# Kernel optimization log

Measured on AMD Instinct MI355X. Metric: run time of the kernel, lower is better.

The kernel has to match this reference:

```python
import jax, jax.numpy as jnp
import numpy as np

V = 50257   # vocab_size
BLK = 2048  # block_size
L = 4       # n_layer
H = 12      # n_head
C = 768     # n_embd
B, T = 2, 2048
EPS = 1e-5


def _ln(x, w):
    # LayerNorm without bias (config.bias=False)
    m = x.mean(-1, keepdims=True)
    v = ((x - m) ** 2).mean(-1, keepdims=True)
    return (x - m) * jax.lax.rsqrt(v + EPS) * w


def setup_inputs() -> dict:
    key = jax.random.key(0)
    ks = jax.random.split(key, 12)
    s = 0.02  # init std, matches _init_weights
    inp = {
        "idx": jax.random.randint(ks[0], (B, T), 0, V),
        "targets": jax.random.randint(ks[1], (B, T), 0, V),
        "wte": jax.random.normal(ks[2], (V, C), jnp.float32) * s,
        "wpe": jax.random.normal(ks[3], (BLK, C), jnp.float32) * s,
        # per-layer stacked params; linear weights stored as [in, out] (x @ W)
        "ln1_w": jnp.ones((L, C), jnp.float32),
        "attn_w": jax.random.normal(ks[4], (L, C, 3 * C), jnp.float32) * s,
        "attn_proj_w": jax.random.normal(ks[5], (L, C, C), jnp.float32) * s,
        "ln2_w": jnp.ones((L, C), jnp.float32),
        "fc_w": jax.random.normal(ks[6], (L, C, 4 * C), jnp.float32) * s,
        "mlp_proj_w": jax.random.normal(ks[7], (L, 4 * C, C), jnp.float32) * s,
        "lnf_w": jnp.ones((C,), jnp.float32),
        "lm_head_w": jax.random.normal(ks[8], (C, V), jnp.float32) * s,
    }
    return inp


def reference(idx, targets, wte, wpe, ln1_w, attn_w, attn_proj_w, ln2_w,
              fc_w, mlp_proj_w, lnf_w, lm_head_w):
    b, t = idx.shape
    hd = C // H
    x = wte[idx] + wpe[:t]  # [B,T,C] (dropout=0.0)
    mask = jnp.tril(jnp.ones((t, t), bool))

    def block(x, p):
        ln1w, Wqkv, Wo, ln2w, Wfc, Wp = p
        h = _ln(x, ln1w)
        qkv = h @ Wqkv  # [B,T,3C]
        q, k, v = jnp.split(qkv, 3, axis=-1)
        to_heads = lambda z: z.reshape(b, t, H, hd).transpose(0, 2, 1, 3)  # [B,H,T,hd]
        q, k, v = to_heads(q), to_heads(k), to_heads(v)
        att = jnp.einsum('bhqd,bhkd->bhqk', q, k) * (1.0 / np.sqrt(hd))
        att = jnp.where(mask, att, -jnp.inf)
        att = jax.nn.softmax(att, axis=-1)
        y = jnp.einsum('bhqk,bhkd->bhqd', att, v)
        y = y.transpose(0, 2, 1, 3).reshape(b, t, C)
        x = x + y @ Wo
        h2 = _ln(x, ln2w)
        x = x + jax.nn.gelu(h2 @ Wfc, approximate=False) @ Wp
        return x, None

    x, _ = jax.lax.scan(block, x, (ln1_w, attn_w, attn_proj_w, ln2_w, fc_w, mlp_proj_w))
    x = _ln(x, lnf_w)
    logits = x @ lm_head_w  # [B,T,V]
    logp = jax.nn.log_softmax(logits, axis=-1)
    loss = -jnp.take_along_axis(logp, targets[..., None], axis=-1).mean()
    return logits, loss
```

## Files before the change

kernel.cpp:

```cpp
#include <hip/hip_runtime.h>
#include <math.h>


#define TT 2048
#define CC 768
#define HH 12
#define HD 64
#define VV 50257
#define BBATCH 2
#define ROWS (BBATCH * TT)
#define LMSTRIP 8192

typedef __attribute__((ext_vector_type(8))) short short8;
typedef __attribute__((ext_vector_type(4))) float floatx4;

typedef const void __attribute__((address_space(1)))* gas1_cvp;
typedef void __attribute__((address_space(3)))* as3_vp;

static __device__ __forceinline__ void gload_lds16(const void* g, void* l) {
  __builtin_amdgcn_global_load_lds(
      (gas1_cvp)(unsigned long long)g,
      (as3_vp)(unsigned int)(unsigned long long)l, 16, 0, 0);
}

static __device__ __forceinline__ ushort f2bf(float x) {
  unsigned u = __float_as_uint(x);
  unsigned r = (u + 0x7fff + ((u >> 16) & 1)) >> 16;
  return (ushort)r;
}
static __device__ __forceinline__ float bf2f(ushort h) {
  return __uint_as_float(((unsigned)h) << 16);
}

static __device__ __forceinline__ void xcd_swizzle(int gx, int gy, int& bx, int& by) {
  int nwg = gx * gy;
  int orig = by * gx + bx;
  int q = nwg >> 3, r = nwg & 7;
  int xcd = orig & 7, local = orig >> 3;
  int wgid = (xcd < r ? xcd * (q + 1) : r * (q + 1) + (xcd - r) * q) + local;
  bx = wgid % gx;
  by = wgid / gx;
}

__global__ void embed_kernel(const int* __restrict__ idx,
                             const float* __restrict__ wte,
                             const float* __restrict__ wpe,
                             float* __restrict__ x) {
  int i = blockIdx.x * blockDim.x + threadIdx.x;
  int row = i / (CC / 4);
  int c4 = (i % (CC / 4)) * 4;
  int t = row % TT;
  int tok = idx[row];
  float4 a = *(const float4*)(wte + (size_t)tok * CC + c4);
  float4 p = *(const float4*)(wpe + (size_t)t * CC + c4);
  float4 o;
  o.x = a.x + p.x; o.y = a.y + p.y; o.z = a.z + p.z; o.w = a.w + p.w;
  *(float4*)(x + (size_t)row * CC + c4) = o;
}

__global__ void ln_split_kernel(const float* __restrict__ x,
                                const float* __restrict__ w,
                                ushort* __restrict__ hhi,
                                ushort* __restrict__ hlo) {
  int wid = threadIdx.x >> 6;
  int lane = threadIdx.x & 63;
  int row = blockIdx.x * 4 + wid;
  const float* xr = x + (size_t)row * CC;
  float v[12];
#pragma unroll
  for (int c = 0; c < 3; c++) {
    float4 t = *(const float4*)(xr + c * 256 + lane * 4);
    v[c * 4 + 0] = t.x; v[c * 4 + 1] = t.y; v[c * 4 + 2] = t.z; v[c * 4 + 3] = t.w;
  }
  float s = 0.f;
#pragma unroll
  for (int i = 0; i < 12; i++) s += v[i];
#pragma unroll
  for (int o = 32; o > 0; o >>= 1) s += __shfl_xor(s, o);
  float mean = s * (1.0f / CC);
  float vs = 0.f;
#pragma unroll
  for (int i = 0; i < 12; i++) { float d = v[i] - mean; vs += d * d; }
#pragma unroll
  for (int o = 32; o > 0; o >>= 1) vs += __shfl_xor(vs, o);
  float rs = rsqrtf(vs * (1.0f / CC) + 1e-5f);
#pragma unroll
  for (int c = 0; c < 3; c++) {
    float4 wv = *(const float4*)(w + c * 256 + lane * 4);
    float r[4];
    r[0] = (v[c * 4 + 0] - mean) * rs * wv.x;
    r[1] = (v[c * 4 + 1] - mean) * rs * wv.y;
    r[2] = (v[c * 4 + 2] - mean) * rs * wv.z;
    r[3] = (v[c * 4 + 3] - mean) * rs * wv.w;
    ushort4 h, l;
    h.x = f2bf(r[0]); l.x = f2bf(r[0] - bf2f(h.x));
    h.y = f2bf(r[1]); l.y = f2bf(r[1] - bf2f(h.y));
    h.z = f2bf(r[2]); l.z = f2bf(r[2] - bf2f(h.z));
    h.w = f2bf(r[3]); l.w = f2bf(r[3] - bf2f(h.w));
    size_t ob = (size_t)row * CC + c * 256 + lane * 4;
    *(ushort4*)(hhi + ob) = h;
    *(ushort4*)(hlo + ob) = l;
  }
}

__global__ void convt_kernel(const float* __restrict__ in, int Ktot, int Ntot,
                             int c0, ushort* __restrict__ oh,
                             ushort* __restrict__ ol) {
  __shared__ float T[32][33];
  const int n0 = blockIdx.x * 32, k0 = blockIdx.y * 32;
  const int tid = threadIdx.x;
  {
    const int kr = tid >> 3, nc = (tid & 7) * 4;
#pragma unroll
    for (int i = 0; i < 4; i++) {
      int gc = c0 + n0 + nc + i;
      float v = 0.f;
      if (gc < Ntot) v = in[(size_t)(k0 + kr) * Ntot + gc];
      T[kr][nc + i] = v;
    }
  }
  __syncthreads();
  const int nr = tid >> 3, kc = (tid & 7) * 4;
  ushort4 h, l;
  float v0 = T[kc + 0][nr], v1 = T[kc + 1][nr], v2 = T[kc + 2][nr], v3 = T[kc + 3][nr];
  h.x = f2bf(v0); l.x = f2bf(v0 - bf2f(h.x));
  h.y = f2bf(v1); l.y = f2bf(v1 - bf2f(h.y));
  h.z = f2bf(v2); l.z = f2bf(v2 - bf2f(h.z));
  h.w = f2bf(v3); l.w = f2bf(v3 - bf2f(h.w));
  size_t ob = (size_t)(n0 + nr) * Ktot + k0 + kc;
  *(ushort4*)(oh + ob) = h;
  *(ushort4*)(ol + ob) = l;
}

template <int EPI, bool NGUARD, bool OSPLIT>
__global__ __launch_bounds__(256, 2) void gemm_bf16x3(
    const ushort* __restrict__ Ah, const ushort* __restrict__ Al,
    const ushort* __restrict__ Bh, const ushort* __restrict__ Bl,
    const float* __restrict__ Res, float* __restrict__ C,
    ushort* __restrict__ Oh, ushort* __restrict__ Ol,
    int K, int ldc, int nvalid) {
  __shared__ ushort S[2][4][128][32];
  const int tid = threadIdx.x;
  int bx = blockIdx.x, by = blockIdx.y;
  xcd_swizzle(gridDim.x, gridDim.y, bx, by);
  const int m0 = by * 128;
  const int n0 = bx * 128;
  const int lane = tid & 63;
  const int wid = tid >> 6;
  const int wr = wid >> 1, wc = wid & 1;
  const int fr = lane & 15, fq = lane >> 4;

  const ushort* gplane = (wid == 0) ? Ah : (wid == 1) ? Al : (wid == 2) ? Bh : Bl;
  const int t0 = (wid < 2) ? m0 : n0;
  const int srow = lane >> 2;
  const int sslot = lane & 3;

  floatx4 acc[4][4] = {};

  auto stage = [&](int buf, int kk) {
#pragma unroll
    for (int i = 0; i < 8; i++) {
      int r = i * 16 + srow;
      int g = sslot ^ ((r >> 1) & 3);
      const ushort* gp = gplane + (size_t)(t0 + r) * K + kk + g * 8;
      gload_lds16((const void*)gp, (void*)&S[buf][wid][i * 16][0]);
    }
  };

  stage(0, 0);
  int cur = 0;
  for (int k0 = 0; k0 < K; k0 += 32) {
    __syncthreads();
    if (k0 + 32 < K) stage(cur ^ 1, k0 + 32);

    short8 fah[4], fal[4], fbh[4], fbl[4];
#pragma unroll
    for (int mi = 0; mi < 4; mi++) {
      int R = wr * 64 + mi * 16 + fr;
      int sw = (fq ^ ((R >> 1) & 3)) * 8;
      fah[mi] = *reinterpret_cast<const short8*>(&S[cur][0][R][sw]);
      fal[mi] = *reinterpret_cast<const short8*>(&S[cur][1][R][sw]);
    }
#pragma unroll
    for (int ni = 0; ni < 4; ni++) {
      int R = wc * 64 + ni * 16 + fr;
      int sw = (fq ^ ((R >> 1) & 3)) * 8;
      fbh[ni] = *reinterpret_cast<const short8*>(&S[cur][2][R][sw]);
      fbl[ni] = *reinterpret_cast<const short8*>(&S[cur][3][R][sw]);
    }
#pragma unroll
    for (int mi = 0; mi < 4; mi++)
#pragma unroll
      for (int ni = 0; ni < 4; ni++) {
        acc[mi][ni] = __builtin_amdgcn_mfma_f32_16x16x32_bf16(fah[mi], fbh[ni], acc[mi][ni], 0, 0, 0);
        acc[mi][ni] = __builtin_amdgcn_mfma_f32_16x16x32_bf16(fah[mi], fbl[ni], acc[mi][ni], 0, 0, 0);
        acc[mi][ni] = __builtin_amdgcn_mfma_f32_16x16x32_bf16(fal[mi], fbh[ni], acc[mi][ni], 0, 0, 0);
      }
    cur ^= 1;
  }

#pragma unroll
  for (int mi = 0; mi < 4; mi++) {
#pragma unroll
    for (int ni = 0; ni < 4; ni++) {
      int col = n0 + wc * 64 + ni * 16 + fr;
      if (!NGUARD || col < nvalid) {
#pragma unroll
        for (int j = 0; j < 4; j++) {
          int row = m0 + wr * 64 + mi * 16 + fq * 4 + j;
          float v = acc[mi][ni][j];
          if (EPI == 1) v += Res[(size_t)row * ldc + col];
          if (EPI == 2) v = 0.5f * v * (1.0f + erff(v * 0.70710678118654752f));
          if (OSPLIT) {
            ushort hi = f2bf(v);
            ushort lo = f2bf(v - bf2f(hi));
            Oh[(size_t)row * ldc + col] = hi;
            Ol[(size_t)row * ldc + col] = lo;
          } else {
            C[(size_t)row * ldc + col] = v;
          }
        }
      }
    }
  }
}

__global__ __launch_bounds__(256) void attn_kernel(const float* __restrict__ qkv,
                                                   ushort* __restrict__ yh,
                                                   ushort* __restrict__ yl) {
  __shared__ float Ks[32][64];
  __shared__ float Vs[32][64];
  const int tid = threadIdx.x;
  const int bh = blockIdx.y;
  const int b = bh / HH, h = bh % HH;
  const int q0 = blockIdx.x * 64;
  const int qi = q0 + (tid >> 2);
  const int c = tid & 3;
  const float* qptr = qkv + ((size_t)(b * TT + qi)) * (3 * CC) + h * HD + c * 16;
  float q[16], o[16];
#pragma unroll
  for (int i = 0; i < 4; i++) {
    float4 t = *(const float4*)(qptr + i * 4);
    q[i * 4] = t.x; q[i * 4 + 1] = t.y; q[i * 4 + 2] = t.z; q[i * 4 + 3] = t.w;
  }
#pragma unroll
  for (int i = 0; i < 16; i++) o[i] = 0.f;
  float m = -INFINITY, l = 0.f;

  const int kr = tid >> 3;
  const int kc = (tid & 7) * 8;
  const size_t kbase = ((size_t)b * TT) * (3 * CC) + CC + h * HD;
  const size_t vbase = kbase + CC;

  for (int ks = 0; ks <= q0 + 63; ks += 32) {
    {
      const float* kp = qkv + kbase + (size_t)(ks + kr) * (3 * CC) + kc;
      float4 t0 = *(const float4*)(kp);
      float4 t1 = *(const float4*)(kp + 4);
      *(float4*)&Ks[kr][kc] = t0;
      *(float4*)&Ks[kr][kc + 4] = t1;
      const float* vp = qkv + vbase + (size_t)(ks + kr) * (3 * CC) + kc;
      float4 t2 = *(const float4*)(vp);
      float4 t3 = *(const float4*)(vp + 4);
      *(float4*)&Vs[kr][kc] = t2;
      *(float4*)&Vs[kr][kc + 4] = t3;
    }
    __syncthreads();
    float s[32];
    float tmax = -INFINITY;
#pragma unroll
    for (int j = 0; j < 32; j++) {
      float acc = 0.f;
#pragma unroll
      for (int d = 0; d < 16; d += 4) {
        float4 kv = *(const float4*)&Ks[j][c * 16 + d];
        acc = fmaf(q[d + 0], kv.x, acc);
        acc = fmaf(q[d + 1], kv.y, acc);
        acc = fmaf(q[d + 2], kv.z, acc);
        acc = fmaf(q[d + 3], kv.w, acc);
      }
      acc += __shfl_xor(acc, 1);
      acc += __shfl_xor(acc, 2);
      acc *= 0.125f;
      if (ks + j > qi) acc = -INFINITY;
      s[j] = acc;
      tmax = fmaxf(tmax, acc);
    }
    if (tmax != -INFINITY) {
      if (tmax > m) {
        float f = __expf(m - tmax);
        l *= f;
#pragma unroll
        for (int d = 0; d < 16; d++) o[d] *= f;
        m = tmax;
      }
      float ps = 0.f;
#pragma unroll
      for (int j = 0; j < 32; j++) {
        float p = __expf(s[j] - m);
        s[j] = p;
        ps += p;
      }
      l += ps;
#pragma unroll
      for (int j = 0; j < 32; j++) {
        float p = s[j];
#pragma unroll
        for (int d = 0; d < 16; d += 4) {
          float4 vv = *(const float4*)&Vs[j][c * 16 + d];
          o[d + 0] = fmaf(p, vv.x, o[d + 0]);
          o[d + 1] = fmaf(p, vv.y, o[d + 1]);
          o[d + 2] = fmaf(p, vv.z, o[d + 2]);
          o[d + 3] = fmaf(p, vv.w, o[d + 3]);
        }
      }
    }
    __syncthreads();
  }
  float inv = 1.0f / l;
  size_t yoff = ((size_t)(b * TT + qi)) * CC + h * HD + c * 16;
#pragma unroll
  for (int d = 0; d < 16; d += 4) {
    ushort4 hv, lv;
    float r0 = o[d + 0] * inv, r1 = o[d + 1] * inv;
    float r2 = o[d + 2] * inv, r3 = o[d + 3] * inv;
    hv.x = f2bf(r0); lv.x = f2bf(r0 - bf2f(hv.x));
    hv.y = f2bf(r1); lv.y = f2bf(r1 - bf2f(hv.y));
    hv.z = f2bf(r2); lv.z = f2bf(r2 - bf2f(hv.z));
    hv.w = f2bf(r3); lv.w = f2bf(r3 - bf2f(hv.w));
    *(ushort4*)(yh + yoff + d) = hv;
    *(ushort4*)(yl + yoff + d) = lv;
  }
}

__global__ void loss_rows_kernel(const float* __restrict__ logits,
                                 const int* __restrict__ tgt,
                                 float* __restrict__ rloss) {
  __shared__ float redm[4], reds[4];
  const int row = blockIdx.x;
  const int tid = threadIdx.x;
  const int wid = tid >> 6, lane = tid & 63;
  const float* lr = logits + (size_t)row * VV;
  float m = -INFINITY, s = 0.f;
  for (int i = tid; i < 12564; i += 256) {
    float4 v = *(const float4*)(lr + 4 * i);
    float mv = fmaxf(fmaxf(v.x, v.y), fmaxf(v.z, v.w));
    float mn = fmaxf(m, mv);
    s = s * __expf(m - mn) + __expf(v.x - mn) + __expf(v.y - mn) +
        __expf(v.z - mn) + __expf(v.w - mn);
    m = mn;
  }
  if (tid == 0) {
    float v = lr[VV - 1];
    float mn = fmaxf(m, v);
    s = s * __expf(m - mn) + __expf(v - mn);
    m = mn;
  }
#pragma unroll
  for (int o = 32; o > 0; o >>= 1) {
    float mo = __shfl_xor(m, o), so = __shfl_xor(s, o);
    float mn = fmaxf(m, mo);
    s = s * __expf(m - mn) + so * __expf(mo - mn);
    m = mn;
  }
  if (lane == 0) { redm[wid] = m; reds[wid] = s; }
  __syncthreads();
  if (tid == 0) {
    float M = redm[0], S = reds[0];
#pragma unroll
    for (int w = 1; w < 4; w++) {
      float mn = fmaxf(M, redm[w]);
      S = S * __expf(M - mn) + reds[w] * __expf(redm[w] - mn);
      M = mn;
    }
    float lt = lr[tgt[row]];
    rloss[row] = -(lt - M - logf(S));
  }
}

__global__ void loss_final_kernel(const float* __restrict__ rloss,
                                  float* __restrict__ out) {
  __shared__ float red[4];
  const int tid = threadIdx.x;
  const int wid = tid >> 6, lane = tid & 63;
  float s = 0.f;
  for (int i = tid; i < ROWS; i += 256) s += rloss[i];
#pragma unroll
  for (int o = 32; o > 0; o >>= 1) s += __shfl_xor(s, o);
  if (lane == 0) red[wid] = s;
  __syncthreads();
  if (tid == 0) out[0] = (red[0] + red[1] + red[2] + red[3]) * (1.0f / ROWS);
}

extern "C" void kernel_launch(void* const* d_in, const int* in_sizes, int n_in,
                              void* d_out, int out_size, void* d_ws, size_t ws_size,
                              hipStream_t stream) {
  const int* idx = (const int*)d_in[0];
  const int* tgt = (const int*)d_in[1];
  const float* wte = (const float*)d_in[2];
  const float* wpe = (const float*)d_in[3];
  const float* ln1w = (const float*)d_in[4];
  const float* attnw = (const float*)d_in[5];
  const float* attnpw = (const float*)d_in[6];
  const float* ln2w = (const float*)d_in[7];
  const float* fcw = (const float*)d_in[8];
  const float* mlppw = (const float*)d_in[9];
  const float* lnfw = (const float*)d_in[10];
  const float* lmw = (const float*)d_in[11];

  float* logits = (float*)d_out;
  float* loss = logits + (size_t)ROWS * VV;

  float* x = (float*)d_ws;
  float* qkvb = x + (size_t)ROWS * CC;
  float* rls = qkvb + (size_t)ROWS * 3 * CC;
  ushort* h_hi = (ushort*)(rls + ROWS);
  ushort* h_lo = h_hi + (size_t)ROWS * CC;
  ushort* fA_hi = h_lo + (size_t)ROWS * CC;
  ushort* fA_lo = fA_hi + (size_t)ROWS * 4 * CC;
  ushort* wb_hi = fA_lo + (size_t)ROWS * 4 * CC;
  ushort* wb_lo = wb_hi + (size_t)LMSTRIP * CC;

  embed_kernel<<<ROWS * CC / 4 / 256, 256, 0, stream>>>(idx, wte, wpe, x);

  for (int l = 0; l < 4; l++) {
    ln_split_kernel<<<ROWS / 4, 256, 0, stream>>>(x, ln1w + (size_t)l * CC, h_hi, h_lo);
    convt_kernel<<<dim3(3 * CC / 32, CC / 32), 256, 0, stream>>>(
        attnw + (size_t)l * CC * 3 * CC, CC, 3 * CC, 0, wb_hi, wb_lo);
    gemm_bf16x3<0, false, false><<<dim3(3 * CC / 128, ROWS / 128), 256, 0, stream>>>(
        h_hi, h_lo, wb_hi, wb_lo, nullptr, qkvb, nullptr, nullptr, CC, 3 * CC, 3 * CC);
    attn_kernel<<<dim3(TT / 64, BBATCH * HH), 256, 0, stream>>>(qkvb, h_hi, h_lo);
    convt_kernel<<<dim3(CC / 32, CC / 32), 256, 0, stream>>>(
        attnpw + (size_t)l * CC * CC, CC, CC, 0, wb_hi, wb_lo);
    gemm_bf16x3<1, false, false><<<dim3(CC / 128, ROWS / 128), 256, 0, stream>>>(
        h_hi, h_lo, wb_hi, wb_lo, x, x, nullptr, nullptr, CC, CC, CC);
    ln_split_kernel<<<ROWS / 4, 256, 0, stream>>>(x, ln2w + (size_t)l * CC, h_hi, h_lo);
    convt_kernel<<<dim3(4 * CC / 32, CC / 32), 256, 0, stream>>>(
        fcw + (size_t)l * CC * 4 * CC, CC, 4 * CC, 0, wb_hi, wb_lo);
    gemm_bf16x3<2, false, true><<<dim3(4 * CC / 128, ROWS / 128), 256, 0, stream>>>(
        h_hi, h_lo, wb_hi, wb_lo, nullptr, nullptr, fA_hi, fA_lo, CC, 4 * CC, 4 * CC);
    convt_kernel<<<dim3(CC / 32, 4 * CC / 32), 256, 0, stream>>>(
        mlppw + (size_t)l * 4 * CC * CC, 4 * CC, CC, 0, wb_hi, wb_lo);
    gemm_bf16x3<1, false, false><<<dim3(CC / 128, ROWS / 128), 256, 0, stream>>>(
        fA_hi, fA_lo, wb_hi, wb_lo, x, x, nullptr, nullptr, 4 * CC, CC, CC);
  }

  ln_split_kernel<<<ROWS / 4, 256, 0, stream>>>(x, lnfw, h_hi, h_lo);

  for (int c0 = 0; c0 < VV; c0 += LMSTRIP) {
    int nt = VV - c0 < LMSTRIP ? VV - c0 : LMSTRIP;
    convt_kernel<<<dim3(LMSTRIP / 32, CC / 32), 256, 0, stream>>>(
        lmw, CC, VV, c0, wb_hi, wb_lo);
    if (nt == LMSTRIP) {
      gemm_bf16x3<0, false, false><<<dim3(LMSTRIP / 128, ROWS / 128), 256, 0, stream>>>(
          h_hi, h_lo, wb_hi, wb_lo, nullptr, logits + c0, nullptr, nullptr, CC, VV, nt);
    } else {
      gemm_bf16x3<0, true, false><<<dim3((nt + 127) / 128, ROWS / 128), 256, 0, stream>>>(
          h_hi, h_lo, wb_hi, wb_lo, nullptr, logits + c0, nullptr, nullptr, CC, VV, nt);
    }
  }

  loss_rows_kernel<<<ROWS, 256, 0, stream>>>(logits, tgt, rls);
  loss_final_kernel<<<1, 256, 0, stream>>>(rls, loss);
}
```

Baseline: 5.706 ms.

## Prefetch attention K/V tiles into registers, reverse block order, reorder MFMA passes

The attention kernel now loads the next K/V tile into registers while computing on the current shared-memory tile, so global-load latency can overlap the dot-product and softmax work. Query blocks are launched in reverse order so the longest causal blocks start first, which should reduce tail imbalance. The GEMM inner loop issues the three split-bf16 MFMA passes as separate sweeps, spacing out dependent accumulations on the same tile. The prefetch holds extra registers live and clamps its row index at the sequence end.

```diff
diff --git a/kernel.cpp b/kernel.cpp
--- a/kernel.cpp
+++ b/kernel.cpp
@@ -191,11 +191,18 @@
 #pragma unroll
     for (int mi = 0; mi < 4; mi++)
 #pragma unroll
-      for (int ni = 0; ni < 4; ni++) {
+      for (int ni = 0; ni < 4; ni++)
         acc[mi][ni] = __builtin_amdgcn_mfma_f32_16x16x32_bf16(fah[mi], fbh[ni], acc[mi][ni], 0, 0, 0);
+#pragma unroll
+    for (int mi = 0; mi < 4; mi++)
+#pragma unroll
+      for (int ni = 0; ni < 4; ni++)
         acc[mi][ni] = __builtin_amdgcn_mfma_f32_16x16x32_bf16(fah[mi], fbl[ni], acc[mi][ni], 0, 0, 0);
+#pragma unroll
+    for (int mi = 0; mi < 4; mi++)
+#pragma unroll
+      for (int ni = 0; ni < 4; ni++)
         acc[mi][ni] = __builtin_amdgcn_mfma_f32_16x16x32_bf16(fal[mi], fbh[ni], acc[mi][ni], 0, 0, 0);
-      }
     cur ^= 1;
   }
 
@@ -233,7 +240,7 @@
   const int tid = threadIdx.x;
   const int bh = blockIdx.y;
   const int b = bh / HH, h = bh % HH;
-  const int q0 = blockIdx.x * 64;
+  const int q0 = (gridDim.x - 1 - blockIdx.x) * 64;
   const int qi = q0 + (tid >> 2);
   const int c = tid & 3;
   const float* qptr = qkv + ((size_t)(b * TT + qi)) * (3 * CC) + h * HD + c * 16;
@@ -252,20 +259,28 @@
   const size_t kbase = ((size_t)b * TT) * (3 * CC) + CC + h * HD;
   const size_t vbase = kbase + CC;
 
+  float4 pk0, pk1, pv0, pv1;
+  auto ldkv = [&](int ks) {
+    int row = ks + kr;
+    if (row > TT - 1) row = TT - 1;
+    const float* kp = qkv + kbase + (size_t)row * (3 * CC) + kc;
+    pk0 = *(const float4*)(kp);
+    pk1 = *(const float4*)(kp + 4);
+    const float* vp = qkv + vbase + (size_t)row * (3 * CC) + kc;
+    pv0 = *(const float4*)(vp);
+    pv1 = *(const float4*)(vp + 4);
+  };
+  ldkv(0);
+
   for (int ks = 0; ks <= q0 + 63; ks += 32) {
-    {
-      const float* kp = qkv + kbase + (size_t)(ks + kr) * (3 * CC) + kc;
-      float4 t0 = *(const float4*)(kp);
-      float4 t1 = *(const float4*)(kp + 4);
-      *(float4*)&Ks[kr][kc] = t0;
-      *(float4*)&Ks[kr][kc + 4] = t1;
-      const float* vp = qkv + vbase + (size_t)(ks + kr) * (3 * CC) + kc;
-      float4 t2 = *(const float4*)(vp);
-      float4 t3 = *(const float4*)(vp + 4);
-      *(float4*)&Vs[kr][kc] = t2;
-      *(float4*)&Vs[kr][kc + 4] = t3;
-    }
     __syncthreads();
+    *(float4*)&Ks[kr][kc] = pk0;
+    *(float4*)&Ks[kr][kc + 4] = pk1;
+    *(float4*)&Vs[kr][kc] = pv0;
+    *(float4*)&Vs[kr][kc + 4] = pv1;
+    if (ks + 32 <= q0 + 63) ldkv(ks + 32);
+    __syncthreads();
+
     float s[32];
     float tmax = -INFINITY;
 #pragma unroll
@@ -315,7 +330,6 @@
         }
       }
     }
-    __syncthreads();
   }
   float inv = 1.0f / l;
   size_t yoff = ((size_t)(b * TT + qi)) * CC + h * HD + c * 16;
```

Measured after the change: 5.629 ms. About the same (-1.4%).
